# Performance work log

Hardware: AMD Instinct MI355X
Metric: run time of the kernel (lower is better)

Reference implementation:

```python
import jax, jax.numpy as jnp
import numpy as np

N = 10000      # nodes
E = 640000     # edges
D = 128        # hidden = in_dim = out_dim
L = 4          # GatedGCN layers
G = 128        # graphs in batch
C = 10         # classes


def setup_inputs() -> dict:
    key = jax.random.key(0)
    ks = jax.random.split(key, 16)
    s = 0.05
    nrm = lambda k, shape: (jax.random.normal(k, shape, jnp.float32) * s)
    inp = {
        "feature": jax.random.normal(ks[0], (N, D), jnp.float32),
        "edge_index": jax.random.randint(ks[1], (2, E), 0, N),
        "batch": jnp.sort(jax.random.randint(ks[2], (N,), 0, G)),
        # embedding_h
        "embed_w": nrm(ks[3], (D, D)), "embed_b": nrm(ks[4], (D,)),
        # per-layer GatedGCN params (stacked over L layers; all dims D->D)
        "Aw": nrm(ks[5], (L, D, D)), "Ab": nrm(ks[6], (L, D)),
        "Bw": nrm(ks[7], (L, D, D)), "Bb": nrm(ks[8], (L, D)),
        "Dw": nrm(ks[9], (L, D, D)), "Db": nrm(ks[10], (L, D)),
        "Ew": nrm(ks[11], (L, D, D)), "Eb": nrm(ks[12], (L, D)),
        "bn_g": jnp.ones((L, D), jnp.float32), "bn_b": jnp.zeros((L, D), jnp.float32),
        # MLPReadout: 128 -> 64 -> 32 -> 10
        "mlp_w0": nrm(ks[13], (D, D // 2)), "mlp_b0": jnp.zeros((D // 2,), jnp.float32),
        "mlp_w1": nrm(ks[14], (D // 2, D // 4)), "mlp_b1": jnp.zeros((D // 4,), jnp.float32),
        "mlp_w2": nrm(ks[15], (D // 4, C)), "mlp_b2": jnp.zeros((C,), jnp.float32),
    }
    return inp


def reference(feature, edge_index, batch, embed_w, embed_b,
              Aw, Ab, Bw, Bb, Dw, Db, Ew, Eb, bn_g, bn_b,
              mlp_w0, mlp_b0, mlp_w1, mlp_b1, mlp_w2, mlp_b2):
    src, dst = edge_index[0], edge_index[1]  # messages flow src -> dst
    n = feature.shape[0]
    h = feature @ embed_w + embed_b  # [N, D]
    for l in range(L):
        Ah = h @ Aw[l] + Ab[l]
        Bh = h @ Bw[l] + Bb[l]
        Dh = h @ Dw[l] + Db[l]
        Eh = h @ Ew[l] + Eb[l]
        sigma = jax.nn.sigmoid(Dh[dst] + Eh[src])                         # [E, D] edge gates
        num = jax.ops.segment_sum(sigma * Bh[src], dst, num_segments=n)   # gated message sum
        den = jax.ops.segment_sum(sigma, dst, num_segments=n) + 1e-6
        h_new = Ah + num / den
        # BatchNorm1d over nodes (training-mode batch statistics)
        mean = jnp.mean(h_new, axis=0)
        var = jnp.var(h_new, axis=0)
        h_new = bn_g[l] * (h_new - mean) * jax.lax.rsqrt(var + 1e-5) + bn_b[l]
        h = h + jax.nn.relu(h_new)  # residual
    # mean readout per graph
    counts = jax.ops.segment_sum(jnp.ones((n,), h.dtype), batch, num_segments=G)
    hg = jax.ops.segment_sum(h, batch, num_segments=G) / jnp.maximum(counts, 1.0)[:, None]
    x = jax.nn.relu(hg @ mlp_w0 + mlp_b0)
    x = jax.nn.relu(x @ mlp_w1 + mlp_b1)
    return x @ mlp_w2 + mlp_b2  # [G, C]
```

## Files before the change

kernel.cpp:

```cpp
#include <hip/hip_runtime.h>
#include <math.h>

#define D 128
#define BM 128
#define BK 32


__global__ void zero_i32_kernel(int* __restrict__ p, int n) {
    int i = blockIdx.x * blockDim.x + threadIdx.x;
    if (i < n) p[i] = 0;
}


__global__ void count_deg_kernel(const int* __restrict__ dst, int* __restrict__ deg, int E) {
    int e = blockIdx.x * blockDim.x + threadIdx.x;
    if (e < E) atomicAdd(&deg[dst[e]], 1);
}

__global__ __launch_bounds__(1024)
void scan_kernel(const int* __restrict__ deg, int* __restrict__ row_ptr,
                 int* __restrict__ fill_ptr, int n) {
    __shared__ int sums[1024];
    int t = threadIdx.x;
    int per = (n + 1023) / 1024;
    int beg = t * per, end = min(n, beg + per);
    int s = 0;
    for (int i = beg; i < end; ++i) s += deg[i];
    sums[t] = s;
    __syncthreads();
    for (int off = 1; off < 1024; off <<= 1) {
        int v = (t >= off) ? sums[t - off] : 0;
        __syncthreads();
        sums[t] += v;
        __syncthreads();
    }
    if (t == 1023) row_ptr[n] = sums[1023];
    int prefix = (t > 0) ? sums[t - 1] : 0;
    for (int i = beg; i < end; ++i) {
        row_ptr[i] = prefix;
        fill_ptr[i] = prefix;
        prefix += deg[i];
    }
}

__global__ void fill_csr_kernel(const int* __restrict__ src, const int* __restrict__ dst,
                                int* __restrict__ fill_ptr, int* __restrict__ csr_src, int E) {
    int e = blockIdx.x * blockDim.x + threadIdx.x;
    if (e < E) {
        int p = atomicAdd(&fill_ptr[dst[e]], 1);
        csr_src[p] = src[e];
    }
}


__global__ __launch_bounds__(256, 2)
void gemm4_kernel(const float* __restrict__ X,
                  const float* __restrict__ W0, const float* __restrict__ B0, float* __restrict__ C0,
                  const float* __restrict__ W1, const float* __restrict__ B1, float* __restrict__ C1,
                  const float* __restrict__ W2, const float* __restrict__ B2, float* __restrict__ C2,
                  const float* __restrict__ W3, const float* __restrict__ B3, float* __restrict__ C3,
                  int M) {
    const float* W; const float* Bv; float* C;
    switch (blockIdx.y) {
        case 0:  W = W0; Bv = B0; C = C0; break;
        case 1:  W = W1; Bv = B1; C = C1; break;
        case 2:  W = W2; Bv = B2; C = C2; break;
        default: W = W3; Bv = B3; C = C3; break;
    }
    __shared__ float Xs[BK][BM + 4];
    __shared__ float Ws[BK][D];

    const int tid = threadIdx.x;
    const int m0  = blockIdx.x * BM;
    const int tn  = tid & 15;
    const int tm  = tid >> 4;
    const int r0  = tm * 8;
    const int c0  = tn * 4;

    const int srow = tid >> 3;
    const int sq   = tid & 7;

    const float4* X4 = (const float4*)X;
    const float4* W4 = (const float4*)W;

    float acc[8][8];
    #pragma unroll
    for (int i = 0; i < 8; ++i)
        #pragma unroll
        for (int j = 0; j < 8; ++j) acc[i][j] = 0.f;

    float4 xr[4], wr[4];
    #pragma unroll
    for (int t = 0; t < 4; ++t) {
        int m = m0 + t * 32 + srow;
        xr[t] = (m < M) ? X4[(size_t)m * 32 + sq] : make_float4(0.f, 0.f, 0.f, 0.f);
        wr[t] = W4[t * 256 + tid];
    }

    for (int c = 0; c < 4; ++c) {
        if (c) __syncthreads();
        #pragma unroll
        for (int t = 0; t < 4; ++t) {
            int row = t * 32 + srow;
            Xs[sq * 4 + 0][row] = xr[t].x;
            Xs[sq * 4 + 1][row] = xr[t].y;
            Xs[sq * 4 + 2][row] = xr[t].z;
            Xs[sq * 4 + 3][row] = xr[t].w;
            ((float4*)Ws)[t * 256 + tid] = wr[t];
        }
        __syncthreads();
        if (c < 3) {
            #pragma unroll
            for (int t = 0; t < 4; ++t) {
                int m = m0 + t * 32 + srow;
                xr[t] = (m < M) ? X4[(size_t)m * 32 + (c + 1) * 8 + sq]
                                : make_float4(0.f, 0.f, 0.f, 0.f);
                wr[t] = W4[(c + 1) * 1024 + t * 256 + tid];
            }
        }
        #pragma unroll
        for (int k = 0; k < BK; ++k) {
            float4 xa = *(const float4*)&Xs[k][r0];
            float4 xb = *(const float4*)&Xs[k][r0 + 4];
            float4 wa = *(const float4*)&Ws[k][c0];
            float4 wb = *(const float4*)&Ws[k][c0 + 64];
            float xv[8] = {xa.x, xa.y, xa.z, xa.w, xb.x, xb.y, xb.z, xb.w};
            float wv[8] = {wa.x, wa.y, wa.z, wa.w, wb.x, wb.y, wb.z, wb.w};
            #pragma unroll
            for (int i = 0; i < 8; ++i)
                #pragma unroll
                for (int j = 0; j < 8; ++j)
                    acc[i][j] = fmaf(xv[i], wv[j], acc[i][j]);
        }
    }

    float4 ba = ((const float4*)Bv)[tn];
    float4 bb = ((const float4*)Bv)[tn + 16];
    float4* C4 = (float4*)C;
    #pragma unroll
    for (int i = 0; i < 8; ++i) {
        int m = m0 + r0 + i;
        if (m < M) {
            float4 oa, ob;
            oa.x = acc[i][0] + ba.x; oa.y = acc[i][1] + ba.y;
            oa.z = acc[i][2] + ba.z; oa.w = acc[i][3] + ba.w;
            ob.x = acc[i][4] + bb.x; ob.y = acc[i][5] + bb.y;
            ob.z = acc[i][6] + bb.z; ob.w = acc[i][7] + bb.w;
            C4[(size_t)m * 32 + tn]      = oa;
            C4[(size_t)m * 32 + 16 + tn] = ob;
        }
    }
}


__global__ __launch_bounds__(256)
void aggregate_kernel(const float* __restrict__ Ah, const float* __restrict__ Bh,
                      const float* __restrict__ Dh, const float* __restrict__ Eh,
                      const int* __restrict__ row_ptr, const int* __restrict__ csr_src,
                      float* __restrict__ tmp, float* __restrict__ stats, int N) {
    const int nl = threadIdx.x >> 5;
    const int g  = threadIdx.x & 31;
    const int node = blockIdx.x * 8 + nl;

    float4 t4 = make_float4(0.f, 0.f, 0.f, 0.f);
    if (node < N) {
        const float4* Dh4 = (const float4*)Dh;
        const float4* Eh4 = (const float4*)Eh;
        const float4* Bh4 = (const float4*)Bh;
        const float4* Ah4 = (const float4*)Ah;
        const float4 dh = Dh4[(size_t)node * 32 + g];
        float4 num = make_float4(0.f, 0.f, 0.f, 0.f);
        float4 den = make_float4(0.f, 0.f, 0.f, 0.f);
        const int beg = row_ptr[node], end = row_ptr[node + 1];
        const float LOG2E = 1.44269504088896340736f;
        for (int i = beg; i < end; ++i) {
            int s = csr_src[i];
            float4 e4 = Eh4[(size_t)s * 32 + g];
            float4 b4 = Bh4[(size_t)s * 32 + g];
            float sx = __builtin_amdgcn_rcpf(1.f + __builtin_amdgcn_exp2f(-(dh.x + e4.x) * LOG2E));
            float sy = __builtin_amdgcn_rcpf(1.f + __builtin_amdgcn_exp2f(-(dh.y + e4.y) * LOG2E));
            float sz = __builtin_amdgcn_rcpf(1.f + __builtin_amdgcn_exp2f(-(dh.z + e4.z) * LOG2E));
            float sw = __builtin_amdgcn_rcpf(1.f + __builtin_amdgcn_exp2f(-(dh.w + e4.w) * LOG2E));
            num.x = fmaf(sx, b4.x, num.x); den.x += sx;
            num.y = fmaf(sy, b4.y, num.y); den.y += sy;
            num.z = fmaf(sz, b4.z, num.z); den.z += sz;
            num.w = fmaf(sw, b4.w, num.w); den.w += sw;
        }
        float4 ah = Ah4[(size_t)node * 32 + g];
        t4.x = ah.x + num.x / (den.x + 1e-6f);
        t4.y = ah.y + num.y / (den.y + 1e-6f);
        t4.z = ah.z + num.z / (den.z + 1e-6f);
        t4.w = ah.w + num.w / (den.w + 1e-6f);
        ((float4*)tmp)[(size_t)node * 32 + g] = t4;
    }

    __shared__ float redV[8][132];
    __shared__ float redQ[8][132];
    *(float4*)&redV[nl][g * 4] = t4;
    float4 q4;
    q4.x = t4.x * t4.x; q4.y = t4.y * t4.y; q4.z = t4.z * t4.z; q4.w = t4.w * t4.w;
    *(float4*)&redQ[nl][g * 4] = q4;
    __syncthreads();
    if (threadIdx.x < 128) {
        int d = threadIdx.x;
        float s = 0.f, s2 = 0.f;
        #pragma unroll
        for (int n2 = 0; n2 < 8; ++n2) { s += redV[n2][d]; s2 += redQ[n2][d]; }
        atomicAdd(&stats[d], s);
        atomicAdd(&stats[D + d], s2);
    }
}


__global__ __launch_bounds__(256)
void bn_apply_kernel(float* __restrict__ h, const float* __restrict__ tmp,
                     const float* __restrict__ stats,
                     const float* __restrict__ gamma, const float* __restrict__ beta,
                     int n) {
    int i = blockIdx.x * blockDim.x + threadIdx.x;
    if (i >= n * 32) return;
    const int d0 = (i & 31) * 4;
    const float inv_n = 1.f / (float)n;
    float4 t4 = ((const float4*)tmp)[i];
    float4 h4 = ((float4*)h)[i];
    float tv[4] = {t4.x, t4.y, t4.z, t4.w};
    float hv[4] = {h4.x, h4.y, h4.z, h4.w};
    #pragma unroll
    for (int j = 0; j < 4; ++j) {
        int d = d0 + j;
        float mean = stats[d] * inv_n;
        float var  = stats[D + d] * inv_n - mean * mean;
        float rs   = rsqrtf(var + 1e-5f);
        float v    = gamma[d] * (tv[j] - mean) * rs + beta[d];
        hv[j] += fmaxf(v, 0.f);
    }
    float4 o; o.x = hv[0]; o.y = hv[1]; o.z = hv[2]; o.w = hv[3];
    ((float4*)h)[i] = o;
}


__device__ inline int lower_bound_i(const int* a, int n, int key) {
    int lo = 0, hi = n;
    while (lo < hi) {
        int mid = (lo + hi) >> 1;
        if (a[mid] < key) lo = mid + 1; else hi = mid;
    }
    return lo;
}

__global__ __launch_bounds__(128)
void readout_kernel(const float* __restrict__ h, const int* __restrict__ batch,
                    float* __restrict__ hg, int n) {
    const int g = blockIdx.x, d = threadIdx.x;
    const int lo = lower_bound_i(batch, n, g);
    const int hi = lower_bound_i(batch, n, g + 1);
    float s = 0.f;
    for (int i = lo; i < hi; ++i) s += h[(size_t)i * D + d];
    float cnt = (float)(hi - lo);
    hg[g * D + d] = s / fmaxf(cnt, 1.f);
}

__global__ __launch_bounds__(128)
void mlp_kernel(const float* __restrict__ hg,
                const float* __restrict__ w0, const float* __restrict__ b0,
                const float* __restrict__ w1, const float* __restrict__ b1,
                const float* __restrict__ w2, const float* __restrict__ b2,
                float* __restrict__ out) {
    const int g = blockIdx.x, t = threadIdx.x;
    __shared__ float x[128], y[64], z[32];
    x[t] = hg[g * 128 + t];
    __syncthreads();
    if (t < 64) {
        float a = b0[t];
        #pragma unroll 8
        for (int k = 0; k < 128; ++k) a = fmaf(x[k], w0[k * 64 + t], a);
        y[t] = fmaxf(a, 0.f);
    }
    __syncthreads();
    if (t < 32) {
        float a = b1[t];
        #pragma unroll 8
        for (int k = 0; k < 64; ++k) a = fmaf(y[k], w1[k * 32 + t], a);
        z[t] = fmaxf(a, 0.f);
    }
    __syncthreads();
    if (t < 10) {
        float a = b2[t];
        #pragma unroll 8
        for (int k = 0; k < 32; ++k) a = fmaf(z[k], w2[k * 10 + t], a);
        out[g * 10 + t] = a;
    }
}


extern "C" void kernel_launch(void* const* d_in, const int* in_sizes, int n_in,
                              void* d_out, int out_size, void* d_ws, size_t ws_size,
                              hipStream_t stream) {
    const float* feature  = (const float*)d_in[0];
    const int*   edge_idx = (const int*)  d_in[1];
    const int*   batch    = (const int*)  d_in[2];
    const float* embed_w  = (const float*)d_in[3];
    const float* embed_b  = (const float*)d_in[4];
    const float* Aw = (const float*)d_in[5];
    const float* Ab = (const float*)d_in[6];
    const float* Bw = (const float*)d_in[7];
    const float* Bb = (const float*)d_in[8];
    const float* Dw = (const float*)d_in[9];
    const float* Db = (const float*)d_in[10];
    const float* Ew = (const float*)d_in[11];
    const float* Eb = (const float*)d_in[12];
    const float* bn_g = (const float*)d_in[13];
    const float* bn_b = (const float*)d_in[14];
    const float* mlp_w0 = (const float*)d_in[15];
    const float* mlp_b0 = (const float*)d_in[16];
    const float* mlp_w1 = (const float*)d_in[17];
    const float* mlp_b1 = (const float*)d_in[18];
    const float* mlp_w2 = (const float*)d_in[19];
    const float* mlp_b2 = (const float*)d_in[20];

    const int N = in_sizes[0] / D;
    const int E = in_sizes[1] / 2;
    const int L = in_sizes[6] / D;
    const int G = out_size / 10;

    const int* src = edge_idx;
    const int* dst = edge_idx + E;

    size_t NF = (size_t)N * D;
    float* h     = (float*)d_ws;
    float* Ah    = h + NF;
    float* Bh    = Ah + NF;
    float* Dh    = Bh + NF;
    float* Ehh   = Dh + NF;
    float* tmp   = Ehh + NF;
    float* hg    = tmp + NF;
    float* statsAll = hg + (size_t)G * D;
    int* deg      = (int*)(statsAll + (size_t)L * 2 * D);
    int* row_ptr  = deg + N;
    int* fill_ptr = row_ptr + (N + 1);
    int* csr_src  = fill_ptr + N;

    int nz = L * 2 * D + N;
    zero_i32_kernel<<<dim3((nz + 255) / 256), dim3(256), 0, stream>>>((int*)statsAll, nz);

    count_deg_kernel<<<dim3((E + 255) / 256), dim3(256), 0, stream>>>(dst, deg, E);
    scan_kernel<<<dim3(1), dim3(1024), 0, stream>>>(deg, row_ptr, fill_ptr, N);
    fill_csr_kernel<<<dim3((E + 255) / 256), dim3(256), 0, stream>>>(src, dst, fill_ptr, csr_src, E);

    const int MB = (N + BM - 1) / BM;

    gemm4_kernel<<<dim3(MB, 1), dim3(256), 0, stream>>>(
        feature,
        embed_w, embed_b, h,  embed_w, embed_b, h,
        embed_w, embed_b, h,  embed_w, embed_b, h, N);

    for (int l = 0; l < L; ++l) {
        const float* wA = Aw + (size_t)l * D * D; const float* bA = Ab + (size_t)l * D;
        const float* wB = Bw + (size_t)l * D * D; const float* bB = Bb + (size_t)l * D;
        const float* wD = Dw + (size_t)l * D * D; const float* bD = Db + (size_t)l * D;
        const float* wE = Ew + (size_t)l * D * D; const float* bE = Eb + (size_t)l * D;
        float* stats = statsAll + (size_t)l * 2 * D;

        gemm4_kernel<<<dim3(MB, 4), dim3(256), 0, stream>>>(
            h, wA, bA, Ah,  wB, bB, Bh,  wD, bD, Dh,  wE, bE, Ehh, N);

        aggregate_kernel<<<dim3((N + 7) / 8), dim3(256), 0, stream>>>(
            Ah, Bh, Dh, Ehh, row_ptr, csr_src, tmp, stats, N);

        bn_apply_kernel<<<dim3((N * 32 + 255) / 256), dim3(256), 0, stream>>>(
            h, tmp, stats, bn_g + (size_t)l * D, bn_b + (size_t)l * D, N);
    }

    readout_kernel<<<dim3(G), dim3(128), 0, stream>>>(h, batch, hg, N);
    mlp_kernel<<<dim3(G), dim3(128), 0, stream>>>(
        hg, mlp_w0, mlp_b0, mlp_w1, mlp_b1, mlp_w2, mlp_b2, (float*)d_out);
}
```

Measured before the change: 769.8 us.

## Map one full wavefront per node in aggregation with shuffled neighbor indices

The aggregation kernel now assigns one 64-lane wavefront per destination node, with each lane handling two features through float2 loads, instead of 32 threads per node with float4. Neighbor source indices are loaded cooperatively, 64 at a time, and broadcast with wave shuffles rather than every lane reloading csr_src per edge. The edge loop is unrolled to keep more gathers in flight. The trade-off is twice as many blocks, half the nodes per block, narrower per-lane loads, and more atomic stat updates per node.

```diff
diff --git a/kernel.cpp b/kernel.cpp
--- a/kernel.cpp
+++ b/kernel.cpp
@@ -158,54 +158,54 @@
                       const float* __restrict__ Dh, const float* __restrict__ Eh,
                       const int* __restrict__ row_ptr, const int* __restrict__ csr_src,
                       float* __restrict__ tmp, float* __restrict__ stats, int N) {
-    const int nl = threadIdx.x >> 5;
-    const int g  = threadIdx.x & 31;
-    const int node = blockIdx.x * 8 + nl;
-
-    float4 t4 = make_float4(0.f, 0.f, 0.f, 0.f);
+    const int wl   = threadIdx.x >> 6;
+    const int lane = threadIdx.x & 63;
+    const int node = blockIdx.x * 4 + wl;
+
+    float2 t2 = make_float2(0.f, 0.f);
     if (node < N) {
-        const float4* Dh4 = (const float4*)Dh;
-        const float4* Eh4 = (const float4*)Eh;
-        const float4* Bh4 = (const float4*)Bh;
-        const float4* Ah4 = (const float4*)Ah;
-        const float4 dh = Dh4[(size_t)node * 32 + g];
-        float4 num = make_float4(0.f, 0.f, 0.f, 0.f);
-        float4 den = make_float4(0.f, 0.f, 0.f, 0.f);
+        const float2* Dh2 = (const float2*)Dh;
+        const float2* Eh2 = (const float2*)Eh;
+        const float2* Bh2 = (const float2*)Bh;
+        const float2* Ah2 = (const float2*)Ah;
+        const float2 dh = Dh2[(size_t)node * 64 + lane];
+        float2 num = make_float2(0.f, 0.f);
+        float2 den = make_float2(0.f, 0.f);
         const int beg = row_ptr[node], end = row_ptr[node + 1];
         const float LOG2E = 1.44269504088896340736f;
-        for (int i = beg; i < end; ++i) {
-            int s = csr_src[i];
-            float4 e4 = Eh4[(size_t)s * 32 + g];
-            float4 b4 = Bh4[(size_t)s * 32 + g];
-            float sx = __builtin_amdgcn_rcpf(1.f + __builtin_amdgcn_exp2f(-(dh.x + e4.x) * LOG2E));
-            float sy = __builtin_amdgcn_rcpf(1.f + __builtin_amdgcn_exp2f(-(dh.y + e4.y) * LOG2E));
-            float sz = __builtin_amdgcn_rcpf(1.f + __builtin_amdgcn_exp2f(-(dh.z + e4.z) * LOG2E));
-            float sw = __builtin_amdgcn_rcpf(1.f + __builtin_amdgcn_exp2f(-(dh.w + e4.w) * LOG2E));
-            num.x = fmaf(sx, b4.x, num.x); den.x += sx;
-            num.y = fmaf(sy, b4.y, num.y); den.y += sy;
-            num.z = fmaf(sz, b4.z, num.z); den.z += sz;
-            num.w = fmaf(sw, b4.w, num.w); den.w += sw;
-        }
-        float4 ah = Ah4[(size_t)node * 32 + g];
-        t4.x = ah.x + num.x / (den.x + 1e-6f);
-        t4.y = ah.y + num.y / (den.y + 1e-6f);
-        t4.z = ah.z + num.z / (den.z + 1e-6f);
-        t4.w = ah.w + num.w / (den.w + 1e-6f);
-        ((float4*)tmp)[(size_t)node * 32 + g] = t4;
-    }
-
-    __shared__ float redV[8][132];
-    __shared__ float redQ[8][132];
-    *(float4*)&redV[nl][g * 4] = t4;
-    float4 q4;
-    q4.x = t4.x * t4.x; q4.y = t4.y * t4.y; q4.z = t4.z * t4.z; q4.w = t4.w * t4.w;
-    *(float4*)&redQ[nl][g * 4] = q4;
+        for (int base = beg; base < end; base += 64) {
+            const int cnt = min(64, end - base);
+            int idx = 0;
+            if (lane < cnt) idx = csr_src[base + lane];
+            #pragma unroll 4
+            for (int j = 0; j < cnt; ++j) {
+                int s = __shfl(idx, j, 64);
+                float2 e2 = Eh2[(size_t)s * 64 + lane];
+                float2 b2 = Bh2[(size_t)s * 64 + lane];
+                float sx = __builtin_amdgcn_rcpf(1.f + __builtin_amdgcn_exp2f(-(dh.x + e2.x) * LOG2E));
+                float sy = __builtin_amdgcn_rcpf(1.f + __builtin_amdgcn_exp2f(-(dh.y + e2.y) * LOG2E));
+                num.x = fmaf(sx, b2.x, num.x); den.x += sx;
+                num.y = fmaf(sy, b2.y, num.y); den.y += sy;
+            }
+        }
+        float2 ah = Ah2[(size_t)node * 64 + lane];
+        t2.x = ah.x + num.x / (den.x + 1e-6f);
+        t2.y = ah.y + num.y / (den.y + 1e-6f);
+        ((float2*)tmp)[(size_t)node * 64 + lane] = t2;
+    }
+
+    __shared__ float redV[4][128];
+    __shared__ float redQ[4][128];
+    redV[wl][lane * 2 + 0] = t2.x;
+    redV[wl][lane * 2 + 1] = t2.y;
+    redQ[wl][lane * 2 + 0] = t2.x * t2.x;
+    redQ[wl][lane * 2 + 1] = t2.y * t2.y;
     __syncthreads();
     if (threadIdx.x < 128) {
         int d = threadIdx.x;
         float s = 0.f, s2 = 0.f;
         #pragma unroll
-        for (int n2 = 0; n2 < 8; ++n2) { s += redV[n2][d]; s2 += redQ[n2][d]; }
+        for (int n2 = 0; n2 < 4; ++n2) { s += redV[n2][d]; s2 += redQ[n2][d]; }
         atomicAdd(&stats[d], s);
         atomicAdd(&stats[D + d], s2);
     }
@@ -364,7 +364,7 @@
         gemm4_kernel<<<dim3(MB, 4), dim3(256), 0, stream>>>(
             h, wA, bA, Ah,  wB, bB, Bh,  wD, bD, Dh,  wE, bE, Ehh, N);
 
-        aggregate_kernel<<<dim3((N + 7) / 8), dim3(256), 0, stream>>>(
+        aggregate_kernel<<<dim3((N + 3) / 4), dim3(256), 0, stream>>>(
             Ah, Bh, Dh, Ehh, row_ptr, csr_src, tmp, stats, N);
 
         bn_apply_kernel<<<dim3((N * 32 + 255) / 256), dim3(256), 0, stream>>>(
```

After: 863.6 us. 1.12x slower.
